# Performance work log

Hardware: AMD Instinct MI355X
Metric: run time of the kernel (lower is better)

## Reference

```python
import jax, jax.numpy as jnp
import numpy as np

D_MODEL = 512
D_STATE = 16
D_CONV = 2
DT_RANK = D_MODEL // 16  # mamba default dt_rank = ceil(d_model/16)
D_INNER = D_MODEL        # expand = 1
B, L = 4, 2048
LN_EPS = 1e-5


def setup_inputs() -> dict:
    key = jax.random.key(0)
    ks = jax.random.split(key, 16)
    s = 0.02
    inp = {
        "x_signal": jax.random.normal(ks[0], (B, L, D_MODEL), jnp.float32),
        "x_stats": jax.random.normal(ks[1], (B, 1, D_MODEL), jnp.float32),
        # GatedCrossAttention params (torch Linear weight layout: (out, in))
        "gW1": jax.random.normal(ks[2], (D_MODEL, 2 * D_MODEL), jnp.float32) * s,
        "gb1": jnp.zeros((D_MODEL,), jnp.float32),
        "gW2": jax.random.normal(ks[3], (1, D_MODEL), jnp.float32) * s,
        "gb2": jnp.zeros((1,), jnp.float32),
        "ln_g": jnp.ones((D_MODEL,), jnp.float32),
        "ln_b": jnp.zeros((D_MODEL,), jnp.float32),
        # Mamba params
        "in_proj_W": jax.random.normal(ks[4], (2 * D_INNER, D_MODEL), jnp.float32) * s,
        "conv_w": jax.random.normal(ks[5], (D_INNER, D_CONV), jnp.float32) * s,
        "conv_b": jnp.zeros((D_INNER,), jnp.float32),
        "x_proj_W": jax.random.normal(ks[6], (DT_RANK + 2 * D_STATE, D_INNER), jnp.float32) * s,
        "dt_proj_W": jax.random.normal(ks[7], (D_INNER, DT_RANK), jnp.float32) * s,
        "dt_proj_b": jnp.full((D_INNER,), -4.6, jnp.float32),  # softplus ~ 0.01
        "A_log": jnp.log(jnp.broadcast_to(jnp.arange(1, D_STATE + 1, dtype=jnp.float32), (D_INNER, D_STATE))),
        "Dp": jnp.ones((D_INNER,), jnp.float32),
        "out_proj_W": jax.random.normal(ks[8], (D_MODEL, D_INNER), jnp.float32) * s,
    }
    return inp


def _silu(x):
    return x * jax.nn.sigmoid(x)


def _forward(x_signal, x_stats, gW1, gb1, gW2, gb2, ln_g, ln_b,
             in_proj_W, conv_w, conv_b, x_proj_W, dt_proj_W, dt_proj_b,
             A_log, Dp, out_proj_W):
    # ---- GatedCrossAttention ----
    xs = jnp.broadcast_to(x_stats, x_signal.shape)           # (B,L,D)
    gi = jnp.concatenate([x_signal, xs], axis=-1)            # (B,L,2D)
    h = jax.nn.relu(gi @ gW1.T + gb1)
    gate = jax.nn.sigmoid(h @ gW2.T + gb2)                   # (B,L,1)
    x = x_signal + gate * xs
    mu = jnp.mean(x, -1, keepdims=True)
    var = jnp.var(x, -1, keepdims=True)
    x = (x - mu) * jax.lax.rsqrt(var + LN_EPS) * ln_g + ln_b  # (B,L,D)

    # ---- Mamba (d_state=16, d_conv=2, expand=1) ----
    xz = x @ in_proj_W.T                                     # (B,L,2*Din)
    u, z = jnp.split(xz, 2, axis=-1)
    # causal depthwise conv1d, kernel size 2
    up = jnp.pad(u, ((0, 0), (D_CONV - 1, 0), (0, 0)))
    uc = conv_b + sum(conv_w[:, k] * up[:, k:k + u.shape[1]] for k in range(D_CONV))
    u = _silu(uc)                                            # (B,L,Din)

    xdbc = u @ x_proj_W.T                                    # (B,L,dt_rank+2N)
    dt = xdbc[..., :DT_RANK]
    Bm = xdbc[..., DT_RANK:DT_RANK + D_STATE]                # (B,L,N)
    Cm = xdbc[..., DT_RANK + D_STATE:]                       # (B,L,N)
    delta = jax.nn.softplus(dt @ dt_proj_W.T + dt_proj_b)    # (B,L,Din)

    A = -jnp.exp(A_log)                                      # (Din,N)
    dA = jnp.exp(delta[..., None] * A)                       # (B,L,Din,N)
    dBu = delta[..., None] * Bm[:, :, None, :] * u[..., None]

    def step(hst, inps):
        dA_t, dBu_t, C_t = inps
        hst = dA_t * hst + dBu_t                             # (B,Din,N)
        y_t = jnp.einsum('bdn,bn->bd', hst, C_t)
        return hst, y_t

    h0 = jnp.zeros((u.shape[0], D_INNER, D_STATE), u.dtype)
    xs_scan = (jnp.swapaxes(dA, 0, 1), jnp.swapaxes(dBu, 0, 1), jnp.swapaxes(Cm, 0, 1))
    _, ys = jax.lax.scan(step, h0, xs_scan)                  # (L,B,Din)
    y = jnp.swapaxes(ys, 0, 1) + Dp * u
    y = y * _silu(z)
    out = y @ out_proj_W.T                                   # (B,L,D)
    # dropout is identity in eval mode
    return out


def reference(x_signal, x_stats, gW1, gb1, gW2, gb2, ln_g, ln_b,
              in_proj_W, conv_w, conv_b, x_proj_W, dt_proj_W, dt_proj_b,
              A_log, Dp, out_proj_W):
    return _forward(x_signal, x_stats, gW1, gb1, gW2, gb2, ln_g, ln_b,
                    in_proj_W, conv_w, conv_b, x_proj_W, dt_proj_W, dt_proj_b,
                    A_log, Dp, out_proj_W)
```

## Files before the change

kernel.cpp:

```cpp
#include <hip/hip_runtime.h>
#include <hip/hip_bf16.h>
#include <math.h>

#define D_MODEL 512
#define D_STATE 16
#define DT_RANK 32
#define D_INNER 512
#define BB 4
#define LL 2048
#define MROWS (BB * LL)
#define LN_EPS 1e-5f
#define CHUNK 32
#define NCH (LL / CHUNK)
#define LOG2E 1.44269504f
#define LN2 0.69314718f

typedef __bf16 bf16x8 __attribute__((ext_vector_type(8)));
typedef float f32x4 __attribute__((ext_vector_type(4)));

__device__ __forceinline__ ushort f2bf(float x) {
  uint u = __float_as_uint(x);
  u = (u + 0x7fffu + ((u >> 16) & 1u)) >> 16;
  return (ushort)u;
}
__device__ __forceinline__ float bf2f(ushort h) {
  return __uint_as_float(((uint)h) << 16);
}
__device__ __forceinline__ void split2(float x, ushort& hi, ushort& lo) {
  hi = f2bf(x);
  lo = f2bf(x - bf2f(hi));
}

__device__ __forceinline__ void gload_lds16(const void* g, void* l) {
  __builtin_amdgcn_global_load_lds(
      (const __attribute__((address_space(1))) uint32_t*)g,
      (__attribute__((address_space(3))) uint32_t*)l, 16, 0, 0);
}

template <int EPI>
__global__ __launch_bounds__(256) void gemm_mfma(const ushort* __restrict__ Ahi,
                                                 const ushort* __restrict__ Alo,
                                                 const ushort* __restrict__ Bhi,
                                                 const ushort* __restrict__ Blo,
                                                 float* __restrict__ C, int ldc, int K,
                                                 int nx, const float* __restrict__ e0) {
  __shared__ ushort sA[2][2][128][32];
  __shared__ ushort sB[2][2][64][32];

  const int tid = threadIdx.x;
  const int lane = tid & 63;
  const int wid = tid >> 6;

  const int nwg = gridDim.x;
  const int q = nwg >> 3;
  const int t = (blockIdx.x & 7) * q + (blockIdx.x >> 3);
  const int bx = t % nx;
  const int by = t / nx;
  const int m0 = by * 128;
  const int n0 = bx * 64;

  const int srow = tid >> 2;
  const int koff = (((tid & 3) ^ ((tid >> 3) & 3)) << 3);
  const ushort* Ah_p = Ahi + (size_t)(m0 + srow) * K + koff;
  const ushort* Al_p = Alo + (size_t)(m0 + srow) * K + koff;
  const ushort* Bh_p = Bhi + (size_t)(n0 + srow) * K + koff;
  const ushort* Bl_p = Blo + (size_t)(n0 + srow) * K + koff;
  const size_t rstep = (size_t)64 * K;
  const int wb = wid * 16;

  const int wr = wid >> 1, wc = wid & 1;
  const int fr = lane & 15;
  const int rcs = (((lane >> 4) ^ ((fr >> 1) & 3)) << 3);

  f32x4 acc[4][2] = {};

  auto STAGE = [&](int bq, int kk) {
    gload_lds16(Ah_p + kk,         &sA[bq][0][wb][0]);
    gload_lds16(Ah_p + kk + rstep, &sA[bq][0][64 + wb][0]);
    gload_lds16(Al_p + kk,         &sA[bq][1][wb][0]);
    gload_lds16(Al_p + kk + rstep, &sA[bq][1][64 + wb][0]);
    gload_lds16(Bh_p + kk,         &sB[bq][0][wb][0]);
    gload_lds16(Bl_p + kk,         &sB[bq][1][wb][0]);
  };

  int cur = 0;
  STAGE(0, 0);
  __syncthreads();

  for (int k0 = 0; k0 < K; k0 += 32) {
    if (k0 + 32 < K) STAGE(cur ^ 1, k0 + 32);
    bf16x8 ah[4], al[4], bh[2], bl[2];
#pragma unroll
    for (int m = 0; m < 4; ++m) {
      const int ar = wr * 64 + m * 16 + fr;
      ah[m] = *(const bf16x8*)&sA[cur][0][ar][rcs];
      al[m] = *(const bf16x8*)&sA[cur][1][ar][rcs];
    }
#pragma unroll
    for (int n = 0; n < 2; ++n) {
      const int br = wc * 32 + n * 16 + fr;
      bh[n] = *(const bf16x8*)&sB[cur][0][br][rcs];
      bl[n] = *(const bf16x8*)&sB[cur][1][br][rcs];
    }
#pragma unroll
    for (int m = 0; m < 4; ++m)
#pragma unroll
      for (int n = 0; n < 2; ++n) {
        acc[m][n] = __builtin_amdgcn_mfma_f32_16x16x32_bf16(ah[m], bh[n],
                                                            acc[m][n], 0, 0, 0);
        acc[m][n] = __builtin_amdgcn_mfma_f32_16x16x32_bf16(ah[m], bl[n],
                                                            acc[m][n], 0, 0, 0);
        acc[m][n] = __builtin_amdgcn_mfma_f32_16x16x32_bf16(al[m], bh[n],
                                                            acc[m][n], 0, 0, 0);
      }
    __syncthreads();
    cur ^= 1;
  }

  const int rbase = (lane >> 4) * 4;
#pragma unroll
  for (int m = 0; m < 4; ++m) {
    const int row0 = m0 + wr * 64 + m * 16 + rbase;
#pragma unroll
    for (int n = 0; n < 2; ++n) {
      const int col = n0 + wc * 32 + n * 16 + fr;
#pragma unroll
      for (int r = 0; r < 4; ++r) {
        float v = acc[m][n][r];
        const int row = row0 + r;
        if (EPI == 1) {
          v += e0[(row >> 11) * D_MODEL + col];
          v = fmaxf(v, 0.f);
        } else if (EPI == 2) {
          const float x = v + e0[col];
          const float e = __builtin_amdgcn_exp2f(-fabsf(x) * LOG2E);
          v = fmaxf(x, 0.f) + __log2f(1.f + e) * LN2;
        }
        C[(size_t)row * ldc + col] = v;
      }
    }
  }
}

__global__ __launch_bounds__(256) void bc_gemm(const ushort* __restrict__ Ahi,
                                               const ushort* __restrict__ Alo,
                                               const ushort* __restrict__ Bhi,
                                               const ushort* __restrict__ Blo,
                                               float* __restrict__ BC) {
  __shared__ ushort sA[2][2][64][32];
  __shared__ ushort sB[2][2][32][32];
  const int K = 512;
  const int tid = threadIdx.x;
  const int lane = tid & 63;
  const int wid = tid >> 6;
  const int m0 = blockIdx.x * 64;

  const int srow = lane >> 2;
  const int koff = (((lane & 3) ^ ((lane >> 3) & 3)) << 3);
  const ushort* Ah_p = Ahi + (size_t)(m0 + wid * 16 + srow) * K + koff;
  const ushort* Al_p = Alo + (size_t)(m0 + wid * 16 + srow) * K + koff;
  const ushort* B_p = ((wid < 2) ? Bhi : Blo) + (size_t)((wid & 1) * 16 + srow) * K + koff;

  const int wr = wid >> 1, wc = wid & 1;
  const int fr = lane & 15;
  const int rcs = (((lane >> 4) ^ ((fr >> 1) & 3)) << 3);

  f32x4 acc[2] = {};

  auto STAGE = [&](int bq, int kk) {
    gload_lds16(Ah_p + kk, &sA[bq][0][wid * 16][0]);
    gload_lds16(Al_p + kk, &sA[bq][1][wid * 16][0]);
    gload_lds16(B_p + kk, &sB[bq][wid >> 1][(wid & 1) * 16][0]);
  };

  int cur = 0;
  STAGE(0, 0);
  __syncthreads();

  for (int k0 = 0; k0 < K; k0 += 32) {
    if (k0 + 32 < K) STAGE(cur ^ 1, k0 + 32);
    bf16x8 ah[2], al[2], bh, bl;
#pragma unroll
    for (int m = 0; m < 2; ++m) {
      const int ar = wr * 32 + m * 16 + fr;
      ah[m] = *(const bf16x8*)&sA[cur][0][ar][rcs];
      al[m] = *(const bf16x8*)&sA[cur][1][ar][rcs];
    }
    const int br = wc * 16 + fr;
    bh = *(const bf16x8*)&sB[cur][0][br][rcs];
    bl = *(const bf16x8*)&sB[cur][1][br][rcs];
#pragma unroll
    for (int m = 0; m < 2; ++m) {
      acc[m] = __builtin_amdgcn_mfma_f32_16x16x32_bf16(ah[m], bh, acc[m], 0, 0, 0);
      acc[m] = __builtin_amdgcn_mfma_f32_16x16x32_bf16(ah[m], bl, acc[m], 0, 0, 0);
      acc[m] = __builtin_amdgcn_mfma_f32_16x16x32_bf16(al[m], bh, acc[m], 0, 0, 0);
    }
    __syncthreads();
    cur ^= 1;
  }

  const int rbase = (lane >> 4) * 4;
  const int col = wc * 16 + fr;
#pragma unroll
  for (int m = 0; m < 2; ++m) {
    const int row0 = m0 + wr * 32 + m * 16 + rbase;
#pragma unroll
    for (int r = 0; r < 4; ++r)
      BC[(size_t)(row0 + r) * 32 + col] = acc[m][r];
  }
}

__global__ __launch_bounds__(256) void split_x(const float* __restrict__ x,
                                               ushort* __restrict__ hi,
                                               ushort* __restrict__ lo) {
  const int i = (blockIdx.x * 256 + threadIdx.x) * 4;
  float4 v = *(const float4*)(x + i);
  ushort h0, l0, h1, l1, h2, l2, h3, l3;
  split2(v.x, h0, l0); split2(v.y, h1, l1); split2(v.z, h2, l2); split2(v.w, h3, l3);
  ushort4 hv = {h0, h1, h2, h3}, lv = {l0, l1, l2, l3};
  *(ushort4*)(hi + i) = hv;
  *(ushort4*)(lo + i) = lv;
}

__global__ __launch_bounds__(128) void split_w(const float* __restrict__ gW1,
                                               const float* __restrict__ ipW,
                                               const float* __restrict__ opW,
                                               ushort* __restrict__ Whi,
                                               ushort* __restrict__ Wlo) {
  const int r = blockIdx.x;
  const int t = threadIdx.x;
  const float* src;
  if (r < 512) src = gW1 + (size_t)r * 1024;
  else if (r < 1536) src = ipW + (size_t)(r - 512) * 512;
  else src = opW + (size_t)(r - 1536) * 512;
  const int i = t * 4;
  float4 v = *(const float4*)(src + i);
  ushort h0, l0, h1, l1, h2, l2, h3, l3;
  split2(v.x, h0, l0); split2(v.y, h1, l1); split2(v.z, h2, l2); split2(v.w, h3, l3);
  ushort4 hv = {h0, h1, h2, h3}, lv = {l0, l1, l2, l3};
  *(ushort4*)(Whi + (size_t)r * 512 + i) = hv;
  *(ushort4*)(Wlo + (size_t)r * 512 + i) = lv;
}

__global__ __launch_bounds__(128) void build_xw(const float* __restrict__ xW,
                                                const float* __restrict__ dtW,
                                                ushort* __restrict__ Whi,
                                                ushort* __restrict__ Wlo) {
  const int j = blockIdx.x;
  const int t = threadIdx.x;
  float v[4] = {0.f, 0.f, 0.f, 0.f};
  if (j < 512) {
    __shared__ float sdt[32];
    if (t < 32) sdt[t] = dtW[j * 32 + t];
    __syncthreads();
    const int k = t * 4;
#pragma unroll 8
    for (int r = 0; r < 32; ++r) {
      const float w = sdt[r];
      const float4 xv = *(const float4*)(xW + r * 512 + k);
      v[0] = fmaf(w, xv.x, v[0]);
      v[1] = fmaf(w, xv.y, v[1]);
      v[2] = fmaf(w, xv.z, v[2]);
      v[3] = fmaf(w, xv.w, v[3]);
    }
  } else {
    const float4 xv = *(const float4*)(xW + (size_t)(32 + j - 512) * 512 + t * 4);
    v[0] = xv.x; v[1] = xv.y; v[2] = xv.z; v[3] = xv.w;
  }
  ushort h[4], l[4];
#pragma unroll
  for (int c = 0; c < 4; ++c) split2(v[c], h[c], l[c]);
  const size_t off = (size_t)(2048 + j) * 512 + t * 4;
  ushort4 hv = {h[0], h[1], h[2], h[3]}, lv = {l[0], l[1], l[2], l[3]};
  *(ushort4*)(Whi + off) = hv;
  *(ushort4*)(Wlo + off) = lv;
}

__global__ __launch_bounds__(512) void c1_kernel(const float* __restrict__ xstats,
                                                 const float* __restrict__ gW1,
                                                 const float* __restrict__ gb1,
                                                 float* __restrict__ c1) {
  const int b = blockIdx.x;
  const int j = threadIdx.x;
  float acc = gb1[j];
  const float* xs = xstats + b * D_MODEL;
  const float* w = gW1 + (size_t)j * (2 * D_MODEL) + D_MODEL;
  for (int k = 0; k < D_MODEL; k += 4) {
    acc = fmaf(xs[k], w[k], acc);
    acc = fmaf(xs[k + 1], w[k + 1], acc);
    acc = fmaf(xs[k + 2], w[k + 2], acc);
    acc = fmaf(xs[k + 3], w[k + 3], acc);
  }
  c1[b * D_MODEL + j] = acc;
}

__device__ __forceinline__ float block_sum(float v, float* sm) {
#pragma unroll
  for (int m = 32; m; m >>= 1) v += __shfl_xor(v, m);
  const int lane = threadIdx.x & 63, w = threadIdx.x >> 6;
  __syncthreads();
  if (!lane) sm[w] = v;
  __syncthreads();
  return sm[0] + sm[1] + sm[2] + sm[3];
}

__global__ __launch_bounds__(256) void gate_ln_kernel(const float* __restrict__ H,
                                                      const float* __restrict__ xsig,
                                                      const float* __restrict__ xstats,
                                                      const float* __restrict__ gW2,
                                                      const float* __restrict__ gb2,
                                                      const float* __restrict__ ln_g,
                                                      const float* __restrict__ ln_b,
                                                      ushort* __restrict__ XNhi,
                                                      ushort* __restrict__ XNlo) {
  __shared__ float red[4];
  const int row = blockIdx.x;
  const int b = row >> 11;
  const int tid = threadIdx.x;
  const size_t rb = (size_t)row * D_MODEL;

  float dotv = 0.f;
  for (int j = tid; j < D_MODEL; j += 256) dotv = fmaf(H[rb + j], gW2[j], dotv);
  const float s = block_sum(dotv, red);
  const float gate = 1.f / (1.f + expf(-(s + gb2[0])));

  float xr[2];
#pragma unroll
  for (int ii = 0; ii < 2; ++ii) {
    const int j = tid + ii * 256;
    xr[ii] = xsig[rb + j] + gate * xstats[b * D_MODEL + j];
  }
  float sv = xr[0] + xr[1];
  const float mu = block_sum(sv, red) * (1.f / D_MODEL);
  float s2 = (xr[0] - mu) * (xr[0] - mu) + (xr[1] - mu) * (xr[1] - mu);
  const float var = block_sum(s2, red) * (1.f / D_MODEL);
  const float inv = rsqrtf(var + LN_EPS);
#pragma unroll
  for (int ii = 0; ii < 2; ++ii) {
    const int j = tid + ii * 256;
    const float v = (xr[ii] - mu) * inv * ln_g[j] + ln_b[j];
    ushort h, l;
    split2(v, h, l);
    XNhi[rb + j] = h;
    XNlo[rb + j] = l;
  }
}

__global__ __launch_bounds__(256) void conv_silu_kernel(const float* __restrict__ XZ,
                                                        const float* __restrict__ conv_w,
                                                        const float* __restrict__ conv_b,
                                                        ushort* __restrict__ Uhi,
                                                        ushort* __restrict__ Ulo) {
  const int row = blockIdx.x;
  const bool first = (row & (LL - 1)) == 0;
  const int tid = threadIdx.x;
#pragma unroll
  for (int ii = 0; ii < 2; ++ii) {
    const int j = tid + ii * 256;
    const float up = first ? 0.f : XZ[(size_t)(row - 1) * (2 * D_INNER) + j];
    const float uc = XZ[(size_t)row * (2 * D_INNER) + j];
    float v = conv_b[j] + conv_w[j * 2 + 0] * up + conv_w[j * 2 + 1] * uc;
    v = v / (1.f + expf(-v));
    ushort h, l;
    split2(v, h, l);
    Uhi[(size_t)row * D_INNER + j] = h;
    Ulo[(size_t)row * D_INNER + j] = l;
  }
}

__global__ __launch_bounds__(256) void scan_part1(const float* __restrict__ DELTA,
                                                  const ushort* __restrict__ Uhi,
                                                  const ushort* __restrict__ Ulo,
                                                  const float* __restrict__ BC,
                                                  const float* __restrict__ A_log,
                                                  float* __restrict__ SLOC,
                                                  float* __restrict__ DSUM) {
  __shared__ __align__(16) float sBC[CHUNK][32];
  const int tid = threadIdx.x;
  const int bid = blockIdx.x;
  const int d = ((bid & 1) << 8) + tid;
  const int c = (bid >> 1) & (NCH - 1);
  const int b = bid >> 7;
  const size_t base = (size_t)b * LL + (size_t)c * CHUNK;

  {
    const int row = tid >> 3, col = (tid & 7) << 2;
    *(float4*)&sBC[row][col] = *(const float4*)(BC + (base + row) * 32 + col);
  }
  float A2[16];
#pragma unroll
  for (int n = 0; n < 16; ++n) A2[n] = -expf(A_log[d * 16 + n]) * LOG2E;
  __syncthreads();

  float S[16];
#pragma unroll
  for (int n = 0; n < 16; ++n) S[n] = 0.f;
  float dsum = 0.f;

#pragma unroll 2
  for (int t = 0; t < CHUNK; ++t) {
    const size_t r = base + t;
    const float delta = DELTA[r * D_INNER + d];
    const float u = bf2f(Uhi[r * D_INNER + d]) + bf2f(Ulo[r * D_INNER + d]);
    dsum += delta;
    const float du = delta * u;
    float Bv[16];
#pragma unroll
    for (int i = 0; i < 4; ++i)
      *(float4*)&Bv[i * 4] = *(const float4*)&sBC[t][i * 4];
#pragma unroll
    for (int n = 0; n < 16; ++n) {
      const float dA = __builtin_amdgcn_exp2f(delta * A2[n]);
      S[n] = fmaf(dA, S[n], du * Bv[n]);
    }
  }
  const size_t ci = ((size_t)b * NCH + c) * D_INNER + d;
#pragma unroll
  for (int i = 0; i < 4; ++i)
    *(float4*)(SLOC + ci * 16 + i * 4) = *(const float4*)&S[i * 4];
  DSUM[ci] = dsum;
}

__global__ __launch_bounds__(256) void scan_combine(const float* __restrict__ SLOC,
                                                    const float* __restrict__ DSUM,
                                                    const float* __restrict__ A_log,
                                                    float* __restrict__ HINIT) {
  const int idx = blockIdx.x * 256 + threadIdx.x;
  const int b = idx >> 13;
  const int d = (idx >> 4) & (D_INNER - 1);
  const int n = idx & 15;
  const float A2 = -expf(A_log[d * D_STATE + n]) * LOG2E;
  float h = 0.f;
#pragma unroll 4
  for (int c = 0; c < NCH; ++c) {
    const size_t ci = ((size_t)b * NCH + c) * D_INNER + d;
    HINIT[ci * 16 + n] = h;
    const float a = __builtin_amdgcn_exp2f(A2 * DSUM[ci]);
    h = fmaf(a, h, SLOC[ci * 16 + n]);
  }
}

__global__ __launch_bounds__(256) void scan_part3(const float* __restrict__ DELTA,
                                                  const ushort* __restrict__ Uhi,
                                                  const ushort* __restrict__ Ulo,
                                                  const float* __restrict__ BC,
                                                  const float* __restrict__ XZ,
                                                  const float* __restrict__ A_log,
                                                  const float* __restrict__ Dp,
                                                  const float* __restrict__ HINIT,
                                                  ushort* __restrict__ Yhi,
                                                  ushort* __restrict__ Ylo) {
  __shared__ __align__(16) float sBC[CHUNK][32];
  const int tid = threadIdx.x;
  const int bid = blockIdx.x;
  const int d = ((bid & 1) << 8) + tid;
  const int c = (bid >> 1) & (NCH - 1);
  const int b = bid >> 7;
  const size_t base = (size_t)b * LL + (size_t)c * CHUNK;

  {
    const int row = tid >> 3, col = (tid & 7) << 2;
    *(float4*)&sBC[row][col] = *(const float4*)(BC + (base + row) * 32 + col);
  }
  float A2[16];
#pragma unroll
  for (int n = 0; n < 16; ++n) A2[n] = -expf(A_log[d * 16 + n]) * LOG2E;
  const float Dpd = Dp[d];

  const size_t ci = ((size_t)b * NCH + c) * D_INNER + d;
  float h[16];
#pragma unroll
  for (int i = 0; i < 4; ++i)
    *(float4*)&h[i * 4] = *(const float4*)(HINIT + ci * 16 + i * 4);
  __syncthreads();

#pragma unroll 2
  for (int t = 0; t < CHUNK; ++t) {
    const size_t r = base + t;
    const float delta = DELTA[r * D_INNER + d];
    const float u = bf2f(Uhi[r * D_INNER + d]) + bf2f(Ulo[r * D_INNER + d]);
    const float z = XZ[r * (2 * D_INNER) + D_INNER + d];
    const float du = delta * u;
    float BCv[32];
#pragma unroll
    for (int i = 0; i < 8; ++i)
      *(float4*)&BCv[i * 4] = *(const float4*)&sBC[t][i * 4];
    float y = 0.f;
#pragma unroll
    for (int n = 0; n < 16; ++n) {
      const float dA = __builtin_amdgcn_exp2f(delta * A2[n]);
      h[n] = fmaf(dA, h[n], du * BCv[n]);
      y = fmaf(h[n], BCv[16 + n], y);
    }
    const float sz = z / (1.f + __builtin_amdgcn_exp2f(-z * LOG2E));
    const float o = (y + Dpd * u) * sz;
    ushort hh, ll;
    split2(o, hh, ll);
    Yhi[r * D_INNER + d] = hh;
    Ylo[r * D_INNER + d] = ll;
  }
}

extern "C" void kernel_launch(void* const* d_in, const int* in_sizes, int n_in,
                              void* d_out, int out_size, void* d_ws, size_t ws_size,
                              hipStream_t stream) {
  const float* x_signal = (const float*)d_in[0];
  const float* x_stats  = (const float*)d_in[1];
  const float* gW1      = (const float*)d_in[2];
  const float* gb1      = (const float*)d_in[3];
  const float* gW2      = (const float*)d_in[4];
  const float* gb2      = (const float*)d_in[5];
  const float* ln_g     = (const float*)d_in[6];
  const float* ln_b     = (const float*)d_in[7];
  const float* in_proj_W = (const float*)d_in[8];
  const float* conv_w   = (const float*)d_in[9];
  const float* conv_b   = (const float*)d_in[10];
  const float* x_proj_W = (const float*)d_in[11];
  const float* dt_proj_W = (const float*)d_in[12];
  const float* dt_proj_b = (const float*)d_in[13];
  const float* A_log    = (const float*)d_in[14];
  const float* Dp       = (const float*)d_in[15];
  const float* out_proj_W = (const float*)d_in[16];
  float* out = (float*)d_out;

  float* ws = (float*)d_ws;
  const size_t NE = (size_t)MROWS * D_MODEL;
  float* H    = ws;
  float* XNf  = H + NE;
  float* XZ   = XNf + NE;
  float* UHL  = XZ + 2 * NE;
  float* BC   = UHL + NE;
  float* C1   = BC + (size_t)MROWS * 32;
  float* SLOC = C1 + BB * D_MODEL;
  float* DSUM = SLOC + (size_t)BB * NCH * D_INNER * D_STATE;
  float* HINIT = DSUM + (size_t)BB * NCH * D_INNER;
  float* WSP  = HINIT + (size_t)BB * NCH * D_INNER * D_STATE;

  ushort* XNhi = (ushort*)XNf;
  ushort* XNlo = XNhi + NE;
  ushort* XShi = (ushort*)XZ;
  ushort* XSlo = XShi + NE;
  ushort* Yhi  = (ushort*)H;
  ushort* Ylo  = Yhi + NE;
  ushort* Uhi  = (ushort*)UHL;
  ushort* Ulo  = Uhi + NE;
  ushort* Whi  = (ushort*)WSP;
  ushort* Wlo  = Whi + (size_t)2592 * 512;
  float* DELTA = XNf;

  split_x<<<dim3(NE / 1024), dim3(256), 0, stream>>>(x_signal, XShi, XSlo);
  split_w<<<dim3(2048), dim3(128), 0, stream>>>(gW1, in_proj_W, out_proj_W, Whi, Wlo);
  build_xw<<<dim3(544), dim3(128), 0, stream>>>(x_proj_W, dt_proj_W, Whi, Wlo);

  c1_kernel<<<dim3(BB), dim3(512), 0, stream>>>(x_stats, gW1, gb1, C1);

  gemm_mfma<1><<<dim3(8 * 64), dim3(256), 0, stream>>>(
      XShi, XSlo, Whi, Wlo, H, D_MODEL, D_MODEL, 8, C1);

  gate_ln_kernel<<<dim3(MROWS), dim3(256), 0, stream>>>(H, x_signal, x_stats, gW2, gb2,
                                                        ln_g, ln_b, XNhi, XNlo);

  gemm_mfma<0><<<dim3(16 * 64), dim3(256), 0, stream>>>(
      XNhi, XNlo, Whi + (size_t)512 * 512, Wlo + (size_t)512 * 512, XZ, 2 * D_INNER,
      D_MODEL, 16, nullptr);

  conv_silu_kernel<<<dim3(MROWS), dim3(256), 0, stream>>>(XZ, conv_w, conv_b, Uhi, Ulo);

  gemm_mfma<2><<<dim3(8 * 64), dim3(256), 0, stream>>>(
      Uhi, Ulo, Whi + (size_t)2048 * 512, Wlo + (size_t)2048 * 512, DELTA, 512,
      D_MODEL, 8, dt_proj_b);

  bc_gemm<<<dim3(MROWS / 64), dim3(256), 0, stream>>>(
      Uhi, Ulo, Whi + (size_t)2560 * 512, Wlo + (size_t)2560 * 512, BC);

  scan_part1<<<dim3(BB * NCH * 2), dim3(256), 0, stream>>>(DELTA, Uhi, Ulo, BC, A_log,
                                                           SLOC, DSUM);
  scan_combine<<<dim3(128), dim3(256), 0, stream>>>(SLOC, DSUM, A_log, HINIT);
  scan_part3<<<dim3(BB * NCH * 2), dim3(256), 0, stream>>>(DELTA, Uhi, Ulo, BC, XZ,
                                                           A_log, Dp, HINIT, Yhi, Ylo);

  gemm_mfma<0><<<dim3(8 * 64), dim3(256), 0, stream>>>(
      Yhi, Ylo, Whi + (size_t)1536 * 512, Wlo + (size_t)1536 * 512, out, D_MODEL,
      D_INNER, 8, nullptr);
}
```

Before: 218.3 us.

## Fuse gate dot-product into first GEMM epilogue and merge weight prep kernels

The first GEMM's epilogue now computes relu(acc+bias)·gW2 per row directly. It reduces each row across lanes with shuffles and atomically adds the partial sums into a per-row gate buffer, so the full hidden matrix H is never written to memory or read back by gate_ln. The two weight-preparation kernels are merged into one launch. The scan chunk size is halved to expose more blocks. The cost is an extra memset, nondeterministic float atomics, and more chunk partials to combine in the scan.

```diff
diff --git a/kernel.cpp b/kernel.cpp
--- a/kernel.cpp
+++ b/kernel.cpp
@@ -10,7 +10,7 @@
 #define LL 2048
 #define MROWS (BB * LL)
 #define LN_EPS 1e-5f
-#define CHUNK 32
+#define CHUNK 16
 #define NCH (LL / CHUNK)
 #define LOG2E 1.44269504f
 #define LN2 0.69314718f
@@ -43,7 +43,9 @@
                                                  const ushort* __restrict__ Bhi,
                                                  const ushort* __restrict__ Blo,
                                                  float* __restrict__ C, int ldc, int K,
-                                                 int nx, const float* __restrict__ e0) {
+                                                 int nx, const float* __restrict__ e0,
+                                                 const float* __restrict__ g2,
+                                                 float* __restrict__ sdot) {
   __shared__ ushort sA[2][2][128][32];
   __shared__ ushort sB[2][2][64][32];
 
@@ -118,25 +120,45 @@
   }
 
   const int rbase = (lane >> 4) * 4;
-#pragma unroll
-  for (int m = 0; m < 4; ++m) {
-    const int row0 = m0 + wr * 64 + m * 16 + rbase;
-#pragma unroll
-    for (int n = 0; n < 2; ++n) {
-      const int col = n0 + wc * 32 + n * 16 + fr;
+  if (EPI == 1) {
+    const int c0 = n0 + wc * 32 + fr;
+    const int c1c = n0 + wc * 32 + 16 + fr;
+    const float g2a = g2[c0];
+    const float g2b = g2[c1c];
+#pragma unroll
+    for (int m = 0; m < 4; ++m) {
 #pragma unroll
       for (int r = 0; r < 4; ++r) {
-        float v = acc[m][n][r];
-        const int row = row0 + r;
-        if (EPI == 1) {
-          v += e0[(row >> 11) * D_MODEL + col];
-          v = fmaxf(v, 0.f);
-        } else if (EPI == 2) {
-          const float x = v + e0[col];
-          const float e = __builtin_amdgcn_exp2f(-fabsf(x) * LOG2E);
-          v = fmaxf(x, 0.f) + __log2f(1.f + e) * LN2;
+        const int row = m0 + wr * 64 + m * 16 + rbase + r;
+        const int bofs = (row >> 11) * D_MODEL;
+        const float v0 = fmaxf(acc[m][0][r] + e0[bofs + c0], 0.f);
+        const float v1 = fmaxf(acc[m][1][r] + e0[bofs + c1c], 0.f);
+        float val = fmaf(v0, g2a, v1 * g2b);
+        val += __shfl_xor(val, 1);
+        val += __shfl_xor(val, 2);
+        val += __shfl_xor(val, 4);
+        val += __shfl_xor(val, 8);
+        if (fr == 0) atomicAdd(&sdot[row], val);
+      }
+    }
+  } else {
+#pragma unroll
+    for (int m = 0; m < 4; ++m) {
+      const int row0 = m0 + wr * 64 + m * 16 + rbase;
+#pragma unroll
+      for (int n = 0; n < 2; ++n) {
+        const int col = n0 + wc * 32 + n * 16 + fr;
+#pragma unroll
+        for (int r = 0; r < 4; ++r) {
+          float v = acc[m][n][r];
+          const int row = row0 + r;
+          if (EPI == 2) {
+            const float x = v + e0[col];
+            const float e = __builtin_amdgcn_exp2f(-fabsf(x) * LOG2E);
+            v = fmaxf(x, 0.f) + __log2f(1.f + e) * LN2;
+          }
+          C[(size_t)row * ldc + col] = v;
         }
-        C[(size_t)row * ldc + col] = v;
       }
     }
   }
@@ -222,55 +244,49 @@
   *(ushort4*)(lo + i) = lv;
 }
 
-__global__ __launch_bounds__(128) void split_w(const float* __restrict__ gW1,
-                                               const float* __restrict__ ipW,
-                                               const float* __restrict__ opW,
-                                               ushort* __restrict__ Whi,
-                                               ushort* __restrict__ Wlo) {
+__global__ __launch_bounds__(128) void prep_w(const float* __restrict__ gW1,
+                                              const float* __restrict__ ipW,
+                                              const float* __restrict__ opW,
+                                              const float* __restrict__ xW,
+                                              const float* __restrict__ dtW,
+                                              ushort* __restrict__ Whi,
+                                              ushort* __restrict__ Wlo) {
   const int r = blockIdx.x;
   const int t = threadIdx.x;
-  const float* src;
-  if (r < 512) src = gW1 + (size_t)r * 1024;
-  else if (r < 1536) src = ipW + (size_t)(r - 512) * 512;
-  else src = opW + (size_t)(r - 1536) * 512;
-  const int i = t * 4;
-  float4 v = *(const float4*)(src + i);
-  ushort h0, l0, h1, l1, h2, l2, h3, l3;
-  split2(v.x, h0, l0); split2(v.y, h1, l1); split2(v.z, h2, l2); split2(v.w, h3, l3);
-  ushort4 hv = {h0, h1, h2, h3}, lv = {l0, l1, l2, l3};
-  *(ushort4*)(Whi + (size_t)r * 512 + i) = hv;
-  *(ushort4*)(Wlo + (size_t)r * 512 + i) = lv;
-}
-
-__global__ __launch_bounds__(128) void build_xw(const float* __restrict__ xW,
-                                                const float* __restrict__ dtW,
-                                                ushort* __restrict__ Whi,
-                                                ushort* __restrict__ Wlo) {
-  const int j = blockIdx.x;
-  const int t = threadIdx.x;
-  float v[4] = {0.f, 0.f, 0.f, 0.f};
-  if (j < 512) {
-    __shared__ float sdt[32];
-    if (t < 32) sdt[t] = dtW[j * 32 + t];
-    __syncthreads();
-    const int k = t * 4;
+  float v[4];
+  if (r < 2048) {
+    const float* src;
+    if (r < 512) src = gW1 + (size_t)r * 1024;
+    else if (r < 1536) src = ipW + (size_t)(r - 512) * 512;
+    else src = opW + (size_t)(r - 1536) * 512;
+    const float4 xv = *(const float4*)(src + t * 4);
+    v[0] = xv.x; v[1] = xv.y; v[2] = xv.z; v[3] = xv.w;
+  } else {
+    const int j = r - 2048;
+    v[0] = v[1] = v[2] = v[3] = 0.f;
+    if (j < 512) {
+      __shared__ float sdt[32];
+      if (t < 32) sdt[t] = dtW[j * 32 + t];
+      __syncthreads();
+      const int k = t * 4;
 #pragma unroll 8
-    for (int r = 0; r < 32; ++r) {
-      const float w = sdt[r];
-      const float4 xv = *(const float4*)(xW + r * 512 + k);
-      v[0] = fmaf(w, xv.x, v[0]);
-      v[1] = fmaf(w, xv.y, v[1]);
-      v[2] = fmaf(w, xv.z, v[2]);
-      v[3] = fmaf(w, xv.w, v[3]);
-    }
-  } else {
-    const float4 xv = *(const float4*)(xW + (size_t)(32 + j - 512) * 512 + t * 4);
-    v[0] = xv.x; v[1] = xv.y; v[2] = xv.z; v[3] = xv.w;
+      for (int rr = 0; rr < 32; ++rr) {
+        const float w = sdt[rr];
+        const float4 xv = *(const float4*)(xW + rr * 512 + k);
+        v[0] = fmaf(w, xv.x, v[0]);
+        v[1] = fmaf(w, xv.y, v[1]);
+        v[2] = fmaf(w, xv.z, v[2]);
+        v[3] = fmaf(w, xv.w, v[3]);
+      }
+    } else {
+      const float4 xv = *(const float4*)(xW + (size_t)(32 + j - 512) * 512 + t * 4);
+      v[0] = xv.x; v[1] = xv.y; v[2] = xv.z; v[3] = xv.w;
+    }
   }
   ushort h[4], l[4];
 #pragma unroll
   for (int c = 0; c < 4; ++c) split2(v[c], h[c], l[c]);
-  const size_t off = (size_t)(2048 + j) * 512 + t * 4;
+  const size_t off = (size_t)r * 512 + t * 4;
   ushort4 hv = {h[0], h[1], h[2], h[3]}, lv = {l[0], l[1], l[2], l[3]};
   *(ushort4*)(Whi + off) = hv;
   *(ushort4*)(Wlo + off) = lv;
@@ -304,10 +320,9 @@
   return sm[0] + sm[1] + sm[2] + sm[3];
 }
 
-__global__ __launch_bounds__(256) void gate_ln_kernel(const float* __restrict__ H,
+__global__ __launch_bounds__(256) void gate_ln_kernel(const float* __restrict__ sdot,
                                                       const float* __restrict__ xsig,
                                                       const float* __restrict__ xstats,
-                                                      const float* __restrict__ gW2,
                                                       const float* __restrict__ gb2,
                                                       const float* __restrict__ ln_g,
                                                       const float* __restrict__ ln_b,
@@ -319,10 +334,7 @@
   const int tid = threadIdx.x;
   const size_t rb = (size_t)row * D_MODEL;
 
-  float dotv = 0.f;
-  for (int j = tid; j < D_MODEL; j += 256) dotv = fmaf(H[rb + j], gW2[j], dotv);
-  const float s = block_sum(dotv, red);
-  const float gate = 1.f / (1.f + expf(-(s + gb2[0])));
+  const float gate = 1.f / (1.f + expf(-(sdot[row] + gb2[0])));
 
   float xr[2];
 #pragma unroll
@@ -380,12 +392,12 @@
   const int bid = blockIdx.x;
   const int d = ((bid & 1) << 8) + tid;
   const int c = (bid >> 1) & (NCH - 1);
-  const int b = bid >> 7;
+  const int b = bid >> 8;
   const size_t base = (size_t)b * LL + (size_t)c * CHUNK;
 
   {
-    const int row = tid >> 3, col = (tid & 7) << 2;
-    *(float4*)&sBC[row][col] = *(const float4*)(BC + (base + row) * 32 + col);
+    const int row = tid >> 4, col = (tid & 15) << 1;
+    *(float2*)&sBC[row][col] = *(const float2*)(BC + (base + row) * 32 + col);
   }
   float A2[16];
 #pragma unroll
@@ -455,12 +467,12 @@
   const int bid = blockIdx.x;
   const int d = ((bid & 1) << 8) + tid;
   const int c = (bid >> 1) & (NCH - 1);
-  const int b = bid >> 7;
+  const int b = bid >> 8;
   const size_t base = (size_t)b * LL + (size_t)c * CHUNK;
 
   {
-    const int row = tid >> 3, col = (tid & 7) << 2;
-    *(float4*)&sBC[row][col] = *(const float4*)(BC + (base + row) * 32 + col);
+    const int row = tid >> 4, col = (tid & 15) << 1;
+    *(float2*)&sBC[row][col] = *(const float2*)(BC + (base + row) * 32 + col);
   }
   float A2[16];
 #pragma unroll
@@ -531,7 +543,8 @@
   float* UHL  = XZ + 2 * NE;
   float* BC   = UHL + NE;
   float* C1   = BC + (size_t)MROWS * 32;
-  float* SLOC = C1 + BB * D_MODEL;
+  float* SGATE = C1 + BB * D_MODEL;
+  float* SLOC = SGATE + MROWS;
   float* DSUM = SLOC + (size_t)BB * NCH * D_INNER * D_STATE;
   float* HINIT = DSUM + (size_t)BB * NCH * D_INNER;
   float* WSP  = HINIT + (size_t)BB * NCH * D_INNER * D_STATE;
@@ -548,27 +561,28 @@
   ushort* Wlo  = Whi + (size_t)2592 * 512;
   float* DELTA = XNf;
 
+  hipMemsetAsync(SGATE, 0, MROWS * sizeof(float), stream);
   split_x<<<dim3(NE / 1024), dim3(256), 0, stream>>>(x_signal, XShi, XSlo);
-  split_w<<<dim3(2048), dim3(128), 0, stream>>>(gW1, in_proj_W, out_proj_W, Whi, Wlo);
-  build_xw<<<dim3(544), dim3(128), 0, stream>>>(x_proj_W, dt_proj_W, Whi, Wlo);
+  prep_w<<<dim3(2592), dim3(128), 0, stream>>>(gW1, in_proj_W, out_proj_W, x_proj_W,
+                                               dt_proj_W, Whi, Wlo);
 
   c1_kernel<<<dim3(BB), dim3(512), 0, stream>>>(x_stats, gW1, gb1, C1);
 
   gemm_mfma<1><<<dim3(8 * 64), dim3(256), 0, stream>>>(
-      XShi, XSlo, Whi, Wlo, H, D_MODEL, D_MODEL, 8, C1);
-
-  gate_ln_kernel<<<dim3(MROWS), dim3(256), 0, stream>>>(H, x_signal, x_stats, gW2, gb2,
-                                                        ln_g, ln_b, XNhi, XNlo);
+      XShi, XSlo, Whi, Wlo, nullptr, 0, D_MODEL, 8, C1, gW2, SGATE);
+
+  gate_ln_kernel<<<dim3(MROWS), dim3(256), 0, stream>>>(SGATE, x_signal, x_stats,
+                                                        gb2, ln_g, ln_b, XNhi, XNlo);
 
   gemm_mfma<0><<<dim3(16 * 64), dim3(256), 0, stream>>>(
       XNhi, XNlo, Whi + (size_t)512 * 512, Wlo + (size_t)512 * 512, XZ, 2 * D_INNER,
-      D_MODEL, 16, nullptr);
+      D_MODEL, 16, nullptr, nullptr, nullptr);
 
   conv_silu_kernel<<<dim3(MROWS), dim3(256), 0, stream>>>(XZ, conv_w, conv_b, Uhi, Ulo);
 
   gemm_mfma<2><<<dim3(8 * 64), dim3(256), 0, stream>>>(
       Uhi, Ulo, Whi + (size_t)2048 * 512, Wlo + (size_t)2048 * 512, DELTA, 512,
-      D_MODEL, 8, dt_proj_b);
+      D_MODEL, 8, dt_proj_b, nullptr, nullptr);
 
   bc_gemm<<<dim3(MROWS / 64), dim3(256), 0, stream>>>(
       Uhi, Ulo, Whi + (size_t)2560 * 512, Wlo + (size_t)2560 * 512, BC);
@@ -581,5 +595,5 @@
 
   gemm_mfma<0><<<dim3(8 * 64), dim3(256), 0, stream>>>(
       Yhi, Ylo, Whi + (size_t)1536 * 512, Wlo + (size_t)1536 * 512, out, D_MODEL,
-      D_INNER, 8, nullptr);
-}
+      D_INNER, 8, nullptr, nullptr, nullptr);
+}
```

New measurement: 219.9 us. No clear change (+0.7%).
